# Kernel optimization log

Hardware: AMD Instinct MI355X
Metric: run time of the kernel (lower is better)

## Reference

```python
import jax, jax.numpy as jnp
import numpy as np

B, L, D, K = 16, 512, 512, 8
D2 = 2 * D
KS = 9
PAD = (KS - 1) // 2
EPS = 1e-5


def _conv_block(x, w, b, g, beta):
    # x: [B, L, D]; conv over time dim with 'same' padding, then LayerNorm over D, ReLU
    y = jax.lax.conv_general_dilated(
        x.transpose(0, 2, 1), w, window_strides=(1,), padding=[(PAD, PAD)],
        dimension_numbers=('NCH', 'OIH', 'NCH'))
    y = y.transpose(0, 2, 1) + b  # [B, L, D]
    mean = jnp.mean(y, axis=-1, keepdims=True)
    var = jnp.var(y, axis=-1, keepdims=True)
    y = (y - mean) * jax.lax.rsqrt(var + EPS) * g + beta
    return jax.nn.relu(y)


def _gru_scan(x, w_ih, w_hh, b_ih, b_hh):
    # x: [B, L, D]; torch GRUCell math, input = concat(x_t, h_{t-1}) per module
    def step(h, x_t):
        p = jnp.concatenate([x_t, h], axis=-1)          # [B, D + D2]
        gi = p @ w_ih.T + b_ih                          # [B, 3*D2]
        gh = h @ w_hh.T + b_hh
        ir, iz, inn = jnp.split(gi, 3, axis=-1)
        hr, hz, hn = jnp.split(gh, 3, axis=-1)
        r = jax.nn.sigmoid(ir + hr)
        z = jax.nn.sigmoid(iz + hz)
        n = jnp.tanh(inn + r * hn)
        h_new = (1.0 - z) * n + z * h
        return h_new, h_new

    h0 = jnp.zeros((x.shape[0], w_hh.shape[1]), x.dtype)
    _, hs = jax.lax.scan(step, h0, x.transpose(1, 0, 2))  # [L, B, D2]
    return hs.transpose(1, 0, 2)                           # [B, L, D2]


def setup_inputs() -> dict:
    key = jax.random.key(0)
    ks = jax.random.split(key, 12)
    n = lambda k, sh, s=0.02: jax.random.normal(k, sh, dtype=jnp.float32) * s
    return {
        'h_text': jax.random.normal(ks[0], (B, L, D), dtype=jnp.float32),
        'conv1_w': n(ks[1], (D, D, KS)), 'conv1_b': jnp.zeros((D,), jnp.float32),
        'ln1_g': jnp.ones((D,), jnp.float32), 'ln1_b': jnp.zeros((D,), jnp.float32),
        'conv2_w': n(ks[2], (D, D, KS)), 'conv2_b': jnp.zeros((D,), jnp.float32),
        'ln2_g': jnp.ones((D,), jnp.float32), 'ln2_b': jnp.zeros((D,), jnp.float32),
        'w_ih': n(ks[3], (3 * D2, D + D2)), 'w_hh': n(ks[4], (3 * D2, D2)),
        'b_ih': jnp.zeros((3 * D2,), jnp.float32), 'b_hh': jnp.zeros((3 * D2,), jnp.float32),
        'mdn_w_w': n(ks[5], (K, D2)), 'mdn_w_b': jnp.zeros((K,), jnp.float32),
        'mdn_sigma_w': n(ks[6], (K * D2, D2)), 'mdn_sigma_b': jnp.zeros((K * D2,), jnp.float32),
        'mdn_mu_w': n(ks[7], (K * D2, D2)), 'mdn_mu_b': jnp.zeros((K * D2,), jnp.float32),
    }


def reference(h_text, conv1_w, conv1_b, ln1_g, ln1_b, conv2_w, conv2_b, ln2_g, ln2_b,
              w_ih, w_hh, b_ih, b_hh, mdn_w_w, mdn_w_b, mdn_sigma_w, mdn_sigma_b,
              mdn_mu_w, mdn_mu_b):
    x = _conv_block(h_text, conv1_w, conv1_b, ln1_g, ln1_b)
    x = _conv_block(x, conv2_w, conv2_b, ln2_g, ln2_b)
    h = _gru_scan(x, w_ih, w_hh, b_ih, b_hh)                 # [B, L, 2D]
    w = jax.nn.softmax(h @ mdn_w_w.T + mdn_w_b, axis=-1)     # [B, L, K]
    sigma = jnp.exp(h @ mdn_sigma_w.T + mdn_sigma_b).reshape(B, L, K, D2)
    mu = (h @ mdn_mu_w.T + mdn_mu_b).reshape(B, L, K, D2)
    return (w, sigma, mu)
```

## Files before the change

kernel.cpp:

```cpp
#include <hip/hip_runtime.h>
#include <hip/hip_bf16.h>
#include <math.h>

#define BB 16
#define LL 512
#define DD 512
#define DD2 1024
#define KMIX 8
#define LPAD 520
#define GRU_KSTEPS 33

typedef __attribute__((ext_vector_type(8))) short short8;
typedef __attribute__((ext_vector_type(4))) float f32x4;
typedef unsigned short ushort;

__device__ __forceinline__ float bf2f(ushort u) {
  union { float f; unsigned i; } v; v.i = ((unsigned)u) << 16; return v.f;
}
__device__ __forceinline__ ushort f2bf(float f) {
  union { float f; unsigned i; } v; v.f = f;
  unsigned i = v.i;
  unsigned r = i + 0x7FFF + ((i >> 16) & 1);
  return (ushort)(r >> 16);
}

__global__ void k_zero_bf16(ushort* p, long n) {
  for (long i = blockIdx.x * 256 + threadIdx.x; i < n; i += (long)gridDim.x * 256) p[i] = 0;
}
__global__ void k_fill_xpad(const float* __restrict__ x, ushort* __restrict__ xp) {
  const long n = (long)BB * LPAD * DD;
  for (long i = blockIdx.x * 256 + threadIdx.x; i < n; i += (long)gridDim.x * 256) {
    int d = (int)(i & 511);
    long rest = i >> 9;
    int p = (int)(rest % LPAD);
    int b = (int)(rest / LPAD);
    float v = 0.f;
    if (p >= 4 && p < 516) v = x[((long)b * LL + (p - 4)) * DD + d];
    xp[i] = f2bf(v);
  }
}
__global__ void k_pack_convw(const float* __restrict__ w, ushort* __restrict__ wp) {
  const long n = (long)DD * DD * 9;
  for (long idx = blockIdx.x * 256 + threadIdx.x; idx < n; idx += (long)gridDim.x * 256) {
    int i = (int)(idx & 511);
    int o = (int)((idx >> 9) & 511);
    int k = (int)(idx >> 18);
    wp[idx] = f2bf(w[((long)o * DD + i) * 9 + k]);
  }
}
__global__ void k_pack_wihx(const float* __restrict__ w_ih, ushort* __restrict__ wp) {
  const long n = (long)3 * DD2 * DD;
  for (long idx = blockIdx.x * 256 + threadIdx.x; idx < n; idx += (long)gridDim.x * 256) {
    int i = (int)(idx & 511);
    int nr = (int)(idx >> 9);
    wp[idx] = f2bf(w_ih[(long)nr * 1536 + i]);
  }
}
__global__ void k_pack_bf16(const float* __restrict__ s, ushort* __restrict__ d, long n) {
  for (long i = blockIdx.x * 256 + threadIdx.x; i < n; i += (long)gridDim.x * 256) d[i] = f2bf(s[i]);
}
__global__ void k_pack_gru(const float* __restrict__ w_ih, const float* __restrict__ w_hh,
                           const float* __restrict__ b_hh, ushort* __restrict__ wp) {
  const long n = (long)64 * 6 * GRU_KSTEPS * 64 * 8;
  for (long idx = blockIdx.x * 256 + threadIdx.x; idx < n; idx += (long)gridDim.x * 256) {
    int j = (int)(idx & 7);
    int lane = (int)((idx >> 3) & 63);
    long r9 = idx >> 9;
    int ks = (int)(r9 % GRU_KSTEPS);
    long tmp = r9 / GRU_KSTEPS;
    int s = (int)(tmp % 6);
    int blk = (int)(tmp / 6);
    int k = ks * 32 + ((lane >> 4) << 3) + j;
    int u = blk * 16 + (lane & 15);
    float v = 0.f;
    if (s < 3) {
      if (k < 1024) v = w_ih[((long)(s * DD2 + u)) * 1536 + 512 + k];
    } else {
      int nr = (s - 3) * DD2 + u;
      if (k < 1024) v = w_hh[(long)nr * DD2 + k];
      else if (k == 1024) v = b_hh[nr];
    }
    wp[idx] = f2bf(v);
  }
}
__global__ void k_init_hbuf(ushort* hb, unsigned* flags) {
  int i = blockIdx.x * 256 + threadIdx.x;
  if (i < 16384) hb[i] = 0;
  if (i < 1024) flags[i] = 0u;
}

template <int MODE, int AMAP>
__global__ __launch_bounds__(256) void gemm128(
    const ushort* __restrict__ A, int lda, long segAoff,
    const ushort* __restrict__ Bt, int ldb, long segBoff,
    int nseg, int kseg, void* __restrict__ Cout, int ldc,
    const float* __restrict__ bias) {
  __shared__ ushort As[128 * 64];
  __shared__ ushort Bs[128 * 64];
  const int tid = threadIdx.x, lane = tid & 63, w = tid >> 6;
  const int wr = w >> 1, wc = w & 1;
  const int m0 = blockIdx.y * 128, n0 = blockIdx.x * 128;

  const ushort* Abase;
  if (AMAP == 1) {
    int b = m0 >> 9, l = m0 & 511;
    Abase = A + ((long)(b * LPAD + l)) * DD;
  } else {
    Abase = A + (long)m0 * lda;
  }
  const ushort* Bbase = Bt + (long)n0 * ldb;

  f32x4 acc[4][4];
#pragma unroll
  for (int i = 0; i < 4; i++)
#pragma unroll
    for (int j = 0; j < 4; j++) acc[i][j] = {0.f, 0.f, 0.f, 0.f};

  for (int seg = 0; seg < nseg; ++seg) {
    const ushort* Aseg = Abase + (long)seg * segAoff;
    const ushort* Bseg = Bbase + (long)seg * segBoff;
    for (int k0 = 0; k0 < kseg; k0 += 64) {
#pragma unroll
      for (int it = 0; it < 4; ++it) {
        int chunk = it * 256 + tid;
        int r = chunk >> 3, cc = chunk & 7;
        int sc = cc ^ (r & 7);
        *(short8*)&As[(size_t)chunk * 8] = *(const short8*)(Aseg + (long)r * lda + k0 + sc * 8);
        *(short8*)&Bs[(size_t)chunk * 8] = *(const short8*)(Bseg + (long)r * ldb + k0 + sc * 8);
      }
      __syncthreads();
#pragma unroll
      for (int kk = 0; kk < 2; ++kk) {
        short8 af[4], bfv[4];
#pragma unroll
        for (int m = 0; m < 4; m++) {
          int row = wr * 64 + m * 16 + (lane & 15);
          int ch = (kk * 4 + (lane >> 4)) ^ (row & 7);
          af[m] = *(const short8*)&As[(size_t)(row * 8 + ch) * 8];
        }
#pragma unroll
        for (int nn = 0; nn < 4; nn++) {
          int row = wc * 64 + nn * 16 + (lane & 15);
          int ch = (kk * 4 + (lane >> 4)) ^ (row & 7);
          bfv[nn] = *(const short8*)&Bs[(size_t)(row * 8 + ch) * 8];
        }
#pragma unroll
        for (int m = 0; m < 4; m++)
#pragma unroll
          for (int nn = 0; nn < 4; nn++)
            acc[m][nn] = __builtin_amdgcn_mfma_f32_16x16x32_bf16(af[m], bfv[nn], acc[m][nn], 0, 0, 0);
      }
      __syncthreads();
    }
  }
  float bvals[4];
#pragma unroll
  for (int nn = 0; nn < 4; nn++) {
    int c = n0 + wc * 64 + nn * 16 + (lane & 15);
    bvals[nn] = bias[c];
  }
#pragma unroll
  for (int m = 0; m < 4; m++) {
    int rbase = m0 + wr * 64 + m * 16 + ((lane >> 4) << 2);
#pragma unroll
    for (int nn = 0; nn < 4; nn++) {
      int c = n0 + wc * 64 + nn * 16 + (lane & 15);
#pragma unroll
      for (int j = 0; j < 4; j++) {
        float v = acc[m][nn][j] + bvals[nn];
        long off = (long)(rbase + j) * ldc + c;
        if (MODE == 0) ((float*)Cout)[off] = v;
        else if (MODE == 1) ((ushort*)Cout)[off] = f2bf(v);
        else if (MODE == 2) ((float*)Cout)[off] = v;
        else if (MODE == 3) ((float*)Cout)[off] = expf(v);
        else {
          int r = rbase + j;
          int bb = r >> 9, tt = r & 511, ss = c >> 10, uu = c & 1023;
          long o2 = ((((long)(tt * 64 + (uu >> 4))) * 3 + ss) << 8) + (bb << 4) + (uu & 15);
          ((ushort*)Cout)[o2] = f2bf(v);
        }
      }
    }
  }
}

template <int DSTPAD>
__global__ __launch_bounds__(256) void ln_relu(
    const float* __restrict__ y, const float* __restrict__ g,
    const float* __restrict__ be, ushort* __restrict__ dst) {
  const int r = blockIdx.x, tid = threadIdx.x;
  float v0 = y[(long)r * DD + tid];
  float v1 = y[(long)r * DD + 256 + tid];
  float s = v0 + v1, sq = v0 * v0 + v1 * v1;
#pragma unroll
  for (int o = 32; o; o >>= 1) { s += __shfl_down(s, o); sq += __shfl_down(sq, o); }
  __shared__ float red[8];
  int w = tid >> 6, lane = tid & 63;
  if (lane == 0) { red[w] = s; red[4 + w] = sq; }
  __syncthreads();
  if (tid == 0) {
    float ts = 0.f, tq = 0.f;
#pragma unroll
    for (int i = 0; i < 4; i++) { ts += red[i]; tq += red[4 + i]; }
    red[0] = ts; red[1] = tq;
  }
  __syncthreads();
  float mean = red[0] * (1.f / 512.f);
  float var = red[1] * (1.f / 512.f) - mean * mean;
  float rs = rsqrtf(var + 1e-5f);
  long dbase;
  if (DSTPAD) { int b = r >> 9, l = r & 511; dbase = ((long)(b * LPAD + l + 4)) * DD; }
  else dbase = (long)r * DD;
  float o0 = fmaxf(0.f, (v0 - mean) * rs * g[tid] + be[tid]);
  float o1 = fmaxf(0.f, (v1 - mean) * rs * g[tid + 256] + be[tid + 256]);
  dst[dbase + tid] = f2bf(o0);
  dst[dbase + 256 + tid] = f2bf(o1);
}

__global__ __launch_bounds__(512, 1) void gru_scan(
    const ushort* __restrict__ Wp, const ushort* __restrict__ gix2,
    const float* __restrict__ b_hh,
    ushort* __restrict__ hbuf, ushort* __restrict__ h_seq,
    unsigned* __restrict__ flags) {
  __shared__ float red[8 * 6 * 256];
  const int tid = threadIdx.x, lane = tid & 63, w = tid >> 6, blk = blockIdx.x;
  const int j_c = w;
  const int u_local = lane & 15;
  const int b = ((lane >> 4) << 2) + (j_c & 3);
  const int u = (blk << 4) + u_local;
  const int lanep = ((blk & 1) * 2 + (u_local >> 3)) * 16 + b;
  const long hout_off = ((long)(blk >> 1) * 64 + lanep) * 8 + (u_local & 7);
  const ushort* wpw = Wp + (long)blk * 6 * GRU_KSTEPS * 512 + (long)lane * 8;
  const float bhr = b_hh[u], bhz = b_hh[DD2 + u], bhn = b_hh[2 * DD2 + u];
  float hold = 0.f;

  short8 wr0[4], wr1[4], wr2[4], wr3[4], wr4[4], wr5[4];
#pragma unroll
  for (int i = 0; i < 4; ++i) {
    const int ks = i * 8 + w;
    wr0[i] = *(const short8*)(wpw + (long)(0 * GRU_KSTEPS + ks) * 512);
    wr1[i] = *(const short8*)(wpw + (long)(1 * GRU_KSTEPS + ks) * 512);
    wr2[i] = *(const short8*)(wpw + (long)(2 * GRU_KSTEPS + ks) * 512);
    wr3[i] = *(const short8*)(wpw + (long)(3 * GRU_KSTEPS + ks) * 512);
    wr4[i] = *(const short8*)(wpw + (long)(4 * GRU_KSTEPS + ks) * 512);
    wr5[i] = *(const short8*)(wpw + (long)(5 * GRU_KSTEPS + ks) * 512);
  }

  const int gofs = (b << 4) + u_local;
  for (int t = 0; t < LL; ++t) {
    float gx_r = 0.f, gx_z = 0.f, gx_n = 0.f;
    if (w < 4) {
      const long gbase = ((long)(t * 64 + blk) * 3) << 8;
      gx_r = bf2f(__builtin_nontemporal_load(gix2 + gbase + gofs));
      gx_z = bf2f(__builtin_nontemporal_load(gix2 + gbase + 256 + gofs));
      gx_n = bf2f(__builtin_nontemporal_load(gix2 + gbase + 512 + gofs));
    }

    if (t > 0) {
      if (w == 0) {
        const unsigned tgt = (unsigned)t;
        while (1) {
          unsigned f = __hip_atomic_load(&flags[lane << 4], __ATOMIC_RELAXED,
                                         __HIP_MEMORY_SCOPE_AGENT);
          if (__all((int)(f >= tgt))) break;
          __builtin_amdgcn_s_sleep(1);
        }
      }
      __syncthreads();
    }

    const ushort* hb = hbuf + ((long)t << 14);
    f32x4 acc0 = {0.f,0.f,0.f,0.f}, acc1 = acc0, acc2 = acc0,
          acc3 = acc0, acc4 = acc0, acc5 = acc0;
#pragma unroll
    for (int i = 0; i < 4; ++i) {
      const int ks = i * 8 + w;
      unsigned long long* ap = (unsigned long long*)(hb + (((long)ks * 64 + lane) << 3));
      union { unsigned long long q[2]; short8 v; } cv;
      cv.q[0] = __hip_atomic_load(ap,     __ATOMIC_RELAXED, __HIP_MEMORY_SCOPE_AGENT);
      cv.q[1] = __hip_atomic_load(ap + 1, __ATOMIC_RELAXED, __HIP_MEMORY_SCOPE_AGENT);
      acc0 = __builtin_amdgcn_mfma_f32_16x16x32_bf16(cv.v, wr0[i], acc0, 0, 0, 0);
      acc1 = __builtin_amdgcn_mfma_f32_16x16x32_bf16(cv.v, wr1[i], acc1, 0, 0, 0);
      acc2 = __builtin_amdgcn_mfma_f32_16x16x32_bf16(cv.v, wr2[i], acc2, 0, 0, 0);
      acc3 = __builtin_amdgcn_mfma_f32_16x16x32_bf16(cv.v, wr3[i], acc3, 0, 0, 0);
      acc4 = __builtin_amdgcn_mfma_f32_16x16x32_bf16(cv.v, wr4[i], acc4, 0, 0, 0);
      acc5 = __builtin_amdgcn_mfma_f32_16x16x32_bf16(cv.v, wr5[i], acc5, 0, 0, 0);
    }
#pragma unroll
    for (int j = 0; j < 4; ++j) {
      red[((w * 6 + 0) << 8) + (j << 6) + lane] = acc0[j];
      red[((w * 6 + 1) << 8) + (j << 6) + lane] = acc1[j];
      red[((w * 6 + 2) << 8) + (j << 6) + lane] = acc2[j];
      red[((w * 6 + 3) << 8) + (j << 6) + lane] = acc3[j];
      red[((w * 6 + 4) << 8) + (j << 6) + lane] = acc4[j];
      red[((w * 6 + 5) << 8) + (j << 6) + lane] = acc5[j];
    }
    __syncthreads();
    ushort h16 = 0;
    if (w < 4) {
      float v0 = 0.f, v1 = 0.f, v2 = 0.f, v3 = 0.f, v4 = 0.f, v5 = 0.f;
#pragma unroll
      for (int wv = 0; wv < 8; ++wv) {
        const int base = ((wv * 6) << 8) + (j_c << 6) + lane;
        v0 += red[base];
        v1 += red[base + 256];
        v2 += red[base + 512];
        v3 += red[base + 768];
        v4 += red[base + 1024];
        v5 += red[base + 1280];
      }
      const float rg = 1.f / (1.f + __expf(-(gx_r + v0 + v3 + bhr)));
      const float zg = 1.f / (1.f + __expf(-(gx_z + v1 + v4 + bhz)));
      const float nx = gx_n + v2 + rg * (v5 + bhn);
      const float ng = 1.f - 2.f / (__expf(2.f * nx) + 1.f);
      const float hn = (1.f - zg) * ng + zg * hold;
      hold = hn;
      h16 = f2bf(hn);
    }
    if (t < LL - 1) {
      if (w < 4)
        __hip_atomic_store(hbuf + (((long)(t + 1)) << 14) + hout_off, h16,
                           __ATOMIC_RELAXED, __HIP_MEMORY_SCOPE_AGENT);
      __syncthreads();
      if (tid == 0)
        __hip_atomic_store(&flags[blk << 4], (unsigned)(t + 1), __ATOMIC_RELAXED,
                           __HIP_MEMORY_SCOPE_AGENT);
    }
    if (w < 4)
      __builtin_nontemporal_store(h16, h_seq + ((long)b * LL + t) * DD2 + u);
  }
}

__global__ __launch_bounds__(256) void w_head(
    const ushort* __restrict__ h_seq, const float* __restrict__ ww,
    const float* __restrict__ wb, float* __restrict__ out) {
  const int tid = threadIdx.x, lane = tid & 63, w = tid >> 6;
  const long r = (long)blockIdx.x * 4 + w;
  float s[KMIX];
#pragma unroll
  for (int k = 0; k < KMIX; k++) s[k] = 0.f;
  for (int u = lane; u < DD2; u += 64) {
    float hv = bf2f(h_seq[r * DD2 + u]);
#pragma unroll
    for (int k = 0; k < KMIX; k++) s[k] += hv * ww[(long)k * DD2 + u];
  }
#pragma unroll
  for (int k = 0; k < KMIX; k++)
#pragma unroll
    for (int o = 32; o; o >>= 1) s[k] += __shfl_xor(s[k], o);
#pragma unroll
  for (int k = 0; k < KMIX; k++) s[k] += wb[k];
  float m = s[0];
#pragma unroll
  for (int k = 1; k < KMIX; k++) m = fmaxf(m, s[k]);
  float esum = 0.f;
#pragma unroll
  for (int k = 0; k < KMIX; k++) { s[k] = expf(s[k] - m); esum += s[k]; }
  float mine = 0.f;
#pragma unroll
  for (int k = 0; k < KMIX; k++) if (lane == k) mine = s[k];
  if (lane < KMIX) out[r * KMIX + lane] = mine / esum;
}

extern "C" void kernel_launch(void* const* d_in, const int* in_sizes, int n_in,
                              void* d_out, int out_size, void* d_ws, size_t ws_size,
                              hipStream_t stream) {
  const float* h_text     = (const float*)d_in[0];
  const float* conv1_w    = (const float*)d_in[1];
  const float* conv1_b    = (const float*)d_in[2];
  const float* ln1_g      = (const float*)d_in[3];
  const float* ln1_b      = (const float*)d_in[4];
  const float* conv2_w    = (const float*)d_in[5];
  const float* conv2_b    = (const float*)d_in[6];
  const float* ln2_g      = (const float*)d_in[7];
  const float* ln2_b      = (const float*)d_in[8];
  const float* w_ih       = (const float*)d_in[9];
  const float* w_hh       = (const float*)d_in[10];
  const float* b_ih       = (const float*)d_in[11];
  const float* b_hh       = (const float*)d_in[12];
  const float* mdn_w_w    = (const float*)d_in[13];
  const float* mdn_w_b    = (const float*)d_in[14];
  const float* mdn_sig_w  = (const float*)d_in[15];
  const float* mdn_sig_b  = (const float*)d_in[16];
  const float* mdn_mu_w   = (const float*)d_in[17];
  const float* mdn_mu_b   = (const float*)d_in[18];
  float* out = (float*)d_out;

  char* ws = (char*)d_ws;
  size_t off = 0;
  auto take = [&](size_t bytes) {
    void* p = ws + off;
    off += (bytes + 255) & ~(size_t)255;
    return p;
  };
  ushort* xpad1  = (ushort*)take((size_t)BB * LPAD * DD * 2);
  ushort* xpad2  = (ushort*)take((size_t)BB * LPAD * DD * 2);
  ushort* wpack1 = (ushort*)take((size_t)DD * DD * 9 * 2);
  ushort* wpack2 = (ushort*)take((size_t)DD * DD * 9 * 2);
  float*  ybuf   = (float*) take((size_t)BB * LL * DD * 4);
  ushort* x2     = (ushort*)take((size_t)BB * LL * DD * 2);
  ushort* wihx   = (ushort*)take((size_t)3 * DD2 * DD * 2);
  ushort* gix    = (ushort*)take((size_t)BB * LL * 3 * DD2 * 2);
  ushort* Wp     = (ushort*)take((size_t)64 * 6 * GRU_KSTEPS * 64 * 8 * 2);
  ushort* hseq   = (ushort*)take((size_t)BB * LL * DD2 * 2);
  ushort* mdnmu  = (ushort*)take((size_t)KMIX * DD2 * DD2 * 2);
  ushort* mdnsg  = (ushort*)take((size_t)KMIX * DD2 * DD2 * 2);
  ushort* hbuf   = (ushort*)take((size_t)512 * 16384 * 2);
  unsigned* flags = (unsigned*)take(64 * 16 * 4);

  const long sigma_off = (long)BB * LL * KMIX;
  const long mu_off    = sigma_off + (long)BB * LL * KMIX * DD2;

  k_fill_xpad<<<2048, 256, 0, stream>>>(h_text, xpad1);
  k_zero_bf16<<<2048, 256, 0, stream>>>(xpad2, (long)BB * LPAD * DD);
  k_pack_convw<<<2048, 256, 0, stream>>>(conv1_w, wpack1);
  k_pack_convw<<<2048, 256, 0, stream>>>(conv2_w, wpack2);
  k_pack_wihx<<<2048, 256, 0, stream>>>(w_ih, wihx);
  k_pack_gru<<<2048, 256, 0, stream>>>(w_ih, w_hh, b_hh, Wp);
  k_pack_bf16<<<2048, 256, 0, stream>>>(mdn_mu_w, mdnmu, (long)KMIX * DD2 * DD2);
  k_pack_bf16<<<2048, 256, 0, stream>>>(mdn_sig_w, mdnsg, (long)KMIX * DD2 * DD2);
  k_init_hbuf<<<64, 256, 0, stream>>>(hbuf, flags);

  gemm128<0, 1><<<dim3(4, 64), 256, 0, stream>>>(xpad1, DD, DD, wpack1, DD, (long)DD * DD, 9, DD,
                                                 ybuf, DD, conv1_b);
  ln_relu<1><<<BB * LL, 256, 0, stream>>>(ybuf, ln1_g, ln1_b, xpad2);

  gemm128<0, 1><<<dim3(4, 64), 256, 0, stream>>>(xpad2, DD, DD, wpack2, DD, (long)DD * DD, 9, DD,
                                                 ybuf, DD, conv2_b);
  ln_relu<0><<<BB * LL, 256, 0, stream>>>(ybuf, ln2_g, ln2_b, x2);

  gemm128<4, 0><<<dim3(24, 64), 256, 0, stream>>>(x2, DD, 0, wihx, DD, 0, 1, DD,
                                                  gix, 3 * DD2, b_ih);

  gru_scan<<<64, 512, 0, stream>>>(Wp, gix, b_hh, hbuf, hseq, flags);

  gemm128<3, 0><<<dim3(64, 64), 256, 0, stream>>>(hseq, DD2, 0, mdnsg, DD2, 0, 1, DD2,
                                                  out + sigma_off, KMIX * DD2, mdn_sig_b);
  gemm128<2, 0><<<dim3(64, 64), 256, 0, stream>>>(hseq, DD2, 0, mdnmu, DD2, 0, 1, DD2,
                                                  out + mu_off, KMIX * DD2, mdn_mu_b);
  w_head<<<BB * LL / 4, 256, 0, stream>>>(hseq, mdn_w_w, mdn_w_b, out);
}
```

Before: 1.932 ms.

## Overlap MDN sigma/mu GEMMs with GRU scan in a persistent fused kernel

Merges the GRU recurrence and the MDN sigma/mu projections into one 256-block kernel. 64 blocks run the scan while the other blocks wait on per-timestep flags and compute 128-row chunks of both projections as soon as those hidden states exist. Each chunk loads the shared A tile once for both weight matrices. This hides most of the projection GEMM time behind the latency-bound scan. The cost is contention for CUs and memory bandwidth with the scan blocks, plus reliance on all 256 blocks being co-resident so the spin waits cannot deadlock.

```diff
diff --git a/kernel.cpp b/kernel.cpp
--- a/kernel.cpp
+++ b/kernel.cpp
@@ -170,9 +170,6 @@
         float v = acc[m][nn][j] + bvals[nn];
         long off = (long)(rbase + j) * ldc + c;
         if (MODE == 0) ((float*)Cout)[off] = v;
-        else if (MODE == 1) ((ushort*)Cout)[off] = f2bf(v);
-        else if (MODE == 2) ((float*)Cout)[off] = v;
-        else if (MODE == 3) ((float*)Cout)[off] = expf(v);
         else {
           int r = rbase + j;
           int bb = r >> 9, tt = r & 511, ss = c >> 10, uu = c & 1023;
@@ -217,117 +214,234 @@
   dst[dbase + 256 + tid] = f2bf(o1);
 }
 
-__global__ __launch_bounds__(512, 1) void gru_scan(
+__device__ __forceinline__ void wait_flags(unsigned need, int tid,
+                                           const unsigned* __restrict__ flags) {
+  if ((tid >> 6) == 0) {
+    while (1) {
+      unsigned f = __hip_atomic_load(&flags[(tid & 63) << 4], __ATOMIC_RELAXED,
+                                     __HIP_MEMORY_SCOPE_AGENT);
+      if (__all((int)(f >= need))) break;
+      __builtin_amdgcn_s_sleep(32);
+    }
+  }
+  __syncthreads();
+}
+
+__device__ void do_pair(int m0, int n0,
+                        const ushort* __restrict__ A,
+                        const ushort* __restrict__ Bsg, const ushort* __restrict__ Bmu,
+                        const float* __restrict__ sg_b, const float* __restrict__ mu_b,
+                        float* __restrict__ Cs, float* __restrict__ Cm,
+                        char* smem, int tid) {
+  ushort* As = (ushort*)smem;
+  ushort* B1 = As + 128 * 64;
+  ushort* B2 = B1 + 128 * 64;
+  const int lane = tid & 63, w = tid >> 6;
+  const int wr = w >> 2, wc = w & 3;
+  const ushort* Abase = A + (long)m0 * DD2;
+  const ushort* Bsb = Bsg + (long)n0 * DD2;
+  const ushort* Bmb = Bmu + (long)n0 * DD2;
+  f32x4 accS[4][2], accM[4][2];
+#pragma unroll
+  for (int m = 0; m < 4; m++)
+#pragma unroll
+    for (int n = 0; n < 2; n++) { accS[m][n] = {0.f,0.f,0.f,0.f}; accM[m][n] = {0.f,0.f,0.f,0.f}; }
+
+  for (int k0 = 0; k0 < DD2; k0 += 64) {
+#pragma unroll
+    for (int it = 0; it < 2; ++it) {
+      int chunk = it * 512 + tid;
+      int r = chunk >> 3, cc = chunk & 7, sc = cc ^ (r & 7);
+      *(short8*)&As[(size_t)chunk * 8] = *(const short8*)(Abase + (long)r * DD2 + k0 + sc * 8);
+      *(short8*)&B1[(size_t)chunk * 8] = *(const short8*)(Bsb + (long)r * DD2 + k0 + sc * 8);
+      *(short8*)&B2[(size_t)chunk * 8] = *(const short8*)(Bmb + (long)r * DD2 + k0 + sc * 8);
+    }
+    __syncthreads();
+#pragma unroll
+    for (int kk = 0; kk < 2; ++kk) {
+      short8 af[4], b1[2], b2[2];
+#pragma unroll
+      for (int m = 0; m < 4; m++) {
+        int row = wr * 64 + m * 16 + (lane & 15);
+        int ch = (kk * 4 + (lane >> 4)) ^ (row & 7);
+        af[m] = *(const short8*)&As[(size_t)(row * 8 + ch) * 8];
+      }
+#pragma unroll
+      for (int n = 0; n < 2; n++) {
+        int row = wc * 32 + n * 16 + (lane & 15);
+        int ch = (kk * 4 + (lane >> 4)) ^ (row & 7);
+        b1[n] = *(const short8*)&B1[(size_t)(row * 8 + ch) * 8];
+        b2[n] = *(const short8*)&B2[(size_t)(row * 8 + ch) * 8];
+      }
+#pragma unroll
+      for (int m = 0; m < 4; m++)
+#pragma unroll
+        for (int n = 0; n < 2; n++) {
+          accS[m][n] = __builtin_amdgcn_mfma_f32_16x16x32_bf16(af[m], b1[n], accS[m][n], 0, 0, 0);
+          accM[m][n] = __builtin_amdgcn_mfma_f32_16x16x32_bf16(af[m], b2[n], accM[m][n], 0, 0, 0);
+        }
+    }
+    __syncthreads();
+  }
+  const int ldc = KMIX * DD2;
+#pragma unroll
+  for (int n = 0; n < 2; n++) {
+    const int c = n0 + wc * 32 + n * 16 + (lane & 15);
+    const float bs = sg_b[c], bm = mu_b[c];
+#pragma unroll
+    for (int m = 0; m < 4; m++) {
+      const int rbase = m0 + wr * 64 + m * 16 + ((lane >> 4) << 2);
+#pragma unroll
+      for (int j = 0; j < 4; j++) {
+        const long off = (long)(rbase + j) * ldc + c;
+        Cs[off] = expf(accS[m][n][j] + bs);
+        Cm[off] = accM[m][n][j] + bm;
+      }
+    }
+  }
+}
+
+__global__ __launch_bounds__(512, 4) void fused_scan_mdn(
     const ushort* __restrict__ Wp, const ushort* __restrict__ gix2,
     const float* __restrict__ b_hh,
     ushort* __restrict__ hbuf, ushort* __restrict__ h_seq,
-    unsigned* __restrict__ flags) {
-  __shared__ float red[8 * 6 * 256];
-  const int tid = threadIdx.x, lane = tid & 63, w = tid >> 6, blk = blockIdx.x;
-  const int j_c = w;
-  const int u_local = lane & 15;
-  const int b = ((lane >> 4) << 2) + (j_c & 3);
-  const int u = (blk << 4) + u_local;
-  const int lanep = ((blk & 1) * 2 + (u_local >> 3)) * 16 + b;
-  const long hout_off = ((long)(blk >> 1) * 64 + lanep) * 8 + (u_local & 7);
-  const ushort* wpw = Wp + (long)blk * 6 * GRU_KSTEPS * 512 + (long)lane * 8;
-  const float bhr = b_hh[u], bhz = b_hh[DD2 + u], bhn = b_hh[2 * DD2 + u];
-  float hold = 0.f;
-
-  short8 wr0[4], wr1[4], wr2[4], wr3[4], wr4[4], wr5[4];
-#pragma unroll
-  for (int i = 0; i < 4; ++i) {
-    const int ks = i * 8 + w;
-    wr0[i] = *(const short8*)(wpw + (long)(0 * GRU_KSTEPS + ks) * 512);
-    wr1[i] = *(const short8*)(wpw + (long)(1 * GRU_KSTEPS + ks) * 512);
-    wr2[i] = *(const short8*)(wpw + (long)(2 * GRU_KSTEPS + ks) * 512);
-    wr3[i] = *(const short8*)(wpw + (long)(3 * GRU_KSTEPS + ks) * 512);
-    wr4[i] = *(const short8*)(wpw + (long)(4 * GRU_KSTEPS + ks) * 512);
-    wr5[i] = *(const short8*)(wpw + (long)(5 * GRU_KSTEPS + ks) * 512);
-  }
-
-  const int gofs = (b << 4) + u_local;
-  for (int t = 0; t < LL; ++t) {
-    float gx_r = 0.f, gx_z = 0.f, gx_n = 0.f;
-    if (w < 4) {
-      const long gbase = ((long)(t * 64 + blk) * 3) << 8;
-      gx_r = bf2f(__builtin_nontemporal_load(gix2 + gbase + gofs));
-      gx_z = bf2f(__builtin_nontemporal_load(gix2 + gbase + 256 + gofs));
-      gx_n = bf2f(__builtin_nontemporal_load(gix2 + gbase + 512 + gofs));
-    }
-
-    if (t > 0) {
-      if (w == 0) {
-        const unsigned tgt = (unsigned)t;
-        while (1) {
-          unsigned f = __hip_atomic_load(&flags[lane << 4], __ATOMIC_RELAXED,
-                                         __HIP_MEMORY_SCOPE_AGENT);
-          if (__all((int)(f >= tgt))) break;
-          __builtin_amdgcn_s_sleep(1);
-        }
-      }
-      __syncthreads();
-    }
-
-    const ushort* hb = hbuf + ((long)t << 14);
-    f32x4 acc0 = {0.f,0.f,0.f,0.f}, acc1 = acc0, acc2 = acc0,
-          acc3 = acc0, acc4 = acc0, acc5 = acc0;
+    unsigned* __restrict__ flags,
+    const ushort* __restrict__ mdnsg, const ushort* __restrict__ mdnmu,
+    const float* __restrict__ sg_b, const float* __restrict__ mu_b,
+    float* __restrict__ outS, float* __restrict__ outM) {
+  __shared__ char smem[49152];
+  const int tid = threadIdx.x;
+
+  if (blockIdx.x < 64) {
+    float* red = (float*)smem;
+    const int lane = tid & 63, w = tid >> 6, blk = blockIdx.x;
+    const int j_c = w;
+    const int u_local = lane & 15;
+    const int b = ((lane >> 4) << 2) + (j_c & 3);
+    const int u = (blk << 4) + u_local;
+    const int lanep = ((blk & 1) * 2 + (u_local >> 3)) * 16 + b;
+    const long hout_off = ((long)(blk >> 1) * 64 + lanep) * 8 + (u_local & 7);
+    const ushort* wpw = Wp + (long)blk * 6 * GRU_KSTEPS * 512 + (long)lane * 8;
+    const float bhr = b_hh[u], bhz = b_hh[DD2 + u], bhn = b_hh[2 * DD2 + u];
+    float hold = 0.f;
+
+    short8 wr0[4], wr1[4], wr2[4], wr3[4], wr4[4], wr5[4];
 #pragma unroll
     for (int i = 0; i < 4; ++i) {
       const int ks = i * 8 + w;
-      unsigned long long* ap = (unsigned long long*)(hb + (((long)ks * 64 + lane) << 3));
-      union { unsigned long long q[2]; short8 v; } cv;
-      cv.q[0] = __hip_atomic_load(ap,     __ATOMIC_RELAXED, __HIP_MEMORY_SCOPE_AGENT);
-      cv.q[1] = __hip_atomic_load(ap + 1, __ATOMIC_RELAXED, __HIP_MEMORY_SCOPE_AGENT);
-      acc0 = __builtin_amdgcn_mfma_f32_16x16x32_bf16(cv.v, wr0[i], acc0, 0, 0, 0);
-      acc1 = __builtin_amdgcn_mfma_f32_16x16x32_bf16(cv.v, wr1[i], acc1, 0, 0, 0);
-      acc2 = __builtin_amdgcn_mfma_f32_16x16x32_bf16(cv.v, wr2[i], acc2, 0, 0, 0);
-      acc3 = __builtin_amdgcn_mfma_f32_16x16x32_bf16(cv.v, wr3[i], acc3, 0, 0, 0);
-      acc4 = __builtin_amdgcn_mfma_f32_16x16x32_bf16(cv.v, wr4[i], acc4, 0, 0, 0);
-      acc5 = __builtin_amdgcn_mfma_f32_16x16x32_bf16(cv.v, wr5[i], acc5, 0, 0, 0);
-    }
-#pragma unroll
-    for (int j = 0; j < 4; ++j) {
-      red[((w * 6 + 0) << 8) + (j << 6) + lane] = acc0[j];
-      red[((w * 6 + 1) << 8) + (j << 6) + lane] = acc1[j];
-      red[((w * 6 + 2) << 8) + (j << 6) + lane] = acc2[j];
-      red[((w * 6 + 3) << 8) + (j << 6) + lane] = acc3[j];
-      red[((w * 6 + 4) << 8) + (j << 6) + lane] = acc4[j];
-      red[((w * 6 + 5) << 8) + (j << 6) + lane] = acc5[j];
+      wr0[i] = *(const short8*)(wpw + (long)(0 * GRU_KSTEPS + ks) * 512);
+      wr1[i] = *(const short8*)(wpw + (long)(1 * GRU_KSTEPS + ks) * 512);
+      wr2[i] = *(const short8*)(wpw + (long)(2 * GRU_KSTEPS + ks) * 512);
+      wr3[i] = *(const short8*)(wpw + (long)(3 * GRU_KSTEPS + ks) * 512);
+      wr4[i] = *(const short8*)(wpw + (long)(4 * GRU_KSTEPS + ks) * 512);
+      wr5[i] = *(const short8*)(wpw + (long)(5 * GRU_KSTEPS + ks) * 512);
+    }
+
+    const int gofs = (b << 4) + u_local;
+    for (int t = 0; t < LL; ++t) {
+      float gx_r = 0.f, gx_z = 0.f, gx_n = 0.f;
+      if (w < 4) {
+        const long gbase = ((long)(t * 64 + blk) * 3) << 8;
+        gx_r = bf2f(__builtin_nontemporal_load(gix2 + gbase + gofs));
+        gx_z = bf2f(__builtin_nontemporal_load(gix2 + gbase + 256 + gofs));
+        gx_n = bf2f(__builtin_nontemporal_load(gix2 + gbase + 512 + gofs));
+      }
+      if (t > 0) {
+        if (w == 0) {
+          const unsigned tgt = (unsigned)t;
+          while (1) {
+            unsigned f = __hip_atomic_load(&flags[lane << 4], __ATOMIC_RELAXED,
+                                           __HIP_MEMORY_SCOPE_AGENT);
+            if (__all((int)(f >= tgt))) break;
+            __builtin_amdgcn_s_sleep(1);
+          }
+        }
+        __syncthreads();
+      }
+
+      const ushort* hb = hbuf + ((long)t << 14);
+      f32x4 acc0 = {0.f,0.f,0.f,0.f}, acc1 = acc0, acc2 = acc0,
+            acc3 = acc0, acc4 = acc0, acc5 = acc0;
+#pragma unroll
+      for (int i = 0; i < 4; ++i) {
+        const int ks = i * 8 + w;
+        unsigned long long* ap = (unsigned long long*)(hb + (((long)ks * 64 + lane) << 3));
+        union { unsigned long long q[2]; short8 v; } cv;
+        cv.q[0] = __hip_atomic_load(ap,     __ATOMIC_RELAXED, __HIP_MEMORY_SCOPE_AGENT);
+        cv.q[1] = __hip_atomic_load(ap + 1, __ATOMIC_RELAXED, __HIP_MEMORY_SCOPE_AGENT);
+        acc0 = __builtin_amdgcn_mfma_f32_16x16x32_bf16(cv.v, wr0[i], acc0, 0, 0, 0);
+        acc1 = __builtin_amdgcn_mfma_f32_16x16x32_bf16(cv.v, wr1[i], acc1, 0, 0, 0);
+        acc2 = __builtin_amdgcn_mfma_f32_16x16x32_bf16(cv.v, wr2[i], acc2, 0, 0, 0);
+        acc3 = __builtin_amdgcn_mfma_f32_16x16x32_bf16(cv.v, wr3[i], acc3, 0, 0, 0);
+        acc4 = __builtin_amdgcn_mfma_f32_16x16x32_bf16(cv.v, wr4[i], acc4, 0, 0, 0);
+        acc5 = __builtin_amdgcn_mfma_f32_16x16x32_bf16(cv.v, wr5[i], acc5, 0, 0, 0);
+      }
+#pragma unroll
+      for (int j = 0; j < 4; ++j) {
+        red[((w * 6 + 0) << 8) + (j << 6) + lane] = acc0[j];
+        red[((w * 6 + 1) << 8) + (j << 6) + lane] = acc1[j];
+        red[((w * 6 + 2) << 8) + (j << 6) + lane] = acc2[j];
+        red[((w * 6 + 3) << 8) + (j << 6) + lane] = acc3[j];
+        red[((w * 6 + 4) << 8) + (j << 6) + lane] = acc4[j];
+        red[((w * 6 + 5) << 8) + (j << 6) + lane] = acc5[j];
+      }
+      __syncthreads();
+      ushort h16 = 0;
+      if (w < 4) {
+        float v0 = 0.f, v1 = 0.f, v2 = 0.f, v3 = 0.f, v4 = 0.f, v5 = 0.f;
+#pragma unroll
+        for (int wv = 0; wv < 8; ++wv) {
+          const int base = ((wv * 6) << 8) + (j_c << 6) + lane;
+          v0 += red[base];
+          v1 += red[base + 256];
+          v2 += red[base + 512];
+          v3 += red[base + 768];
+          v4 += red[base + 1024];
+          v5 += red[base + 1280];
+        }
+        const float rg = 1.f / (1.f + __expf(-(gx_r + v0 + v3 + bhr)));
+        const float zg = 1.f / (1.f + __expf(-(gx_z + v1 + v4 + bhz)));
+        const float nx = gx_n + v2 + rg * (v5 + bhn);
+        const float ng = 1.f - 2.f / (__expf(2.f * nx) + 1.f);
+        const float hn = (1.f - zg) * ng + zg * hold;
+        hold = hn;
+        h16 = f2bf(hn);
+      }
+      if (t < LL - 1) {
+        if (w < 4)
+          __hip_atomic_store(hbuf + (((long)(t + 1)) << 14) + hout_off, h16,
+                             __ATOMIC_RELAXED, __HIP_MEMORY_SCOPE_AGENT);
+        __syncthreads();
+        if (tid == 0)
+          __hip_atomic_store(&flags[blk << 4], (unsigned)(t + 1), __ATOMIC_RELAXED,
+                             __HIP_MEMORY_SCOPE_AGENT);
+      }
+      if (w < 4)
+        __hip_atomic_store(h_seq + ((long)b * LL + t) * DD2 + u, h16,
+                           __ATOMIC_RELAXED, __HIP_MEMORY_SCOPE_AGENT);
     }
     __syncthreads();
-    ushort h16 = 0;
-    if (w < 4) {
-      float v0 = 0.f, v1 = 0.f, v2 = 0.f, v3 = 0.f, v4 = 0.f, v5 = 0.f;
-#pragma unroll
-      for (int wv = 0; wv < 8; ++wv) {
-        const int base = ((wv * 6) << 8) + (j_c << 6) + lane;
-        v0 += red[base];
-        v1 += red[base + 256];
-        v2 += red[base + 512];
-        v3 += red[base + 768];
-        v4 += red[base + 1024];
-        v5 += red[base + 1280];
-      }
-      const float rg = 1.f / (1.f + __expf(-(gx_r + v0 + v3 + bhr)));
-      const float zg = 1.f / (1.f + __expf(-(gx_z + v1 + v4 + bhz)));
-      const float nx = gx_n + v2 + rg * (v5 + bhn);
-      const float ng = 1.f - 2.f / (__expf(2.f * nx) + 1.f);
-      const float hn = (1.f - zg) * ng + zg * hold;
-      hold = hn;
-      h16 = f2bf(hn);
-    }
-    if (t < LL - 1) {
-      if (w < 4)
-        __hip_atomic_store(hbuf + (((long)(t + 1)) << 14) + hout_off, h16,
-                           __ATOMIC_RELAXED, __HIP_MEMORY_SCOPE_AGENT);
-      __syncthreads();
-      if (tid == 0)
-        __hip_atomic_store(&flags[blk << 4], (unsigned)(t + 1), __ATOMIC_RELAXED,
-                           __HIP_MEMORY_SCOPE_AGENT);
-    }
-    if (w < 4)
-      __builtin_nontemporal_store(h16, h_seq + ((long)b * LL + t) * DD2 + u);
+    if (tid == 0)
+      __hip_atomic_store(&flags[blk << 4], 600u, __ATOMIC_RELAXED,
+                         __HIP_MEMORY_SCOPE_AGENT);
+  } else {
+    const int wid = blockIdx.x - 64;
+    for (int i = wid; i < 3072; i += 192) {
+      const int nb = i & 63;
+      const int rest = i >> 6;
+      const int b = rest & 15;
+      const int t0 = (rest >> 4) * 128;
+      wait_flags((unsigned)(t0 + 129), tid, flags);
+      do_pair(b * 512 + t0, nb * 128, h_seq, mdnsg, mdnmu, sg_b, mu_b,
+              outS, outM, smem, tid);
+    }
+  }
+  for (int i = blockIdx.x; i < 1024; i += 256) {
+    const int nb = i & 63;
+    const int b = (i >> 6) & 15;
+    wait_flags(513u, tid, flags);
+    do_pair(b * 512 + 384, nb * 128, h_seq, mdnsg, mdnmu, sg_b, mu_b,
+            outS, outM, smem, tid);
   }
 }
 
@@ -432,11 +546,9 @@
   gemm128<4, 0><<<dim3(24, 64), 256, 0, stream>>>(x2, DD, 0, wihx, DD, 0, 1, DD,
                                                   gix, 3 * DD2, b_ih);
 
-  gru_scan<<<64, 512, 0, stream>>>(Wp, gix, b_hh, hbuf, hseq, flags);
-
-  gemm128<3, 0><<<dim3(64, 64), 256, 0, stream>>>(hseq, DD2, 0, mdnsg, DD2, 0, 1, DD2,
-                                                  out + sigma_off, KMIX * DD2, mdn_sig_b);
-  gemm128<2, 0><<<dim3(64, 64), 256, 0, stream>>>(hseq, DD2, 0, mdnmu, DD2, 0, 1, DD2,
-                                                  out + mu_off, KMIX * DD2, mdn_mu_b);
+  fused_scan_mdn<<<256, 512, 0, stream>>>(Wp, gix, b_hh, hbuf, hseq, flags,
+                                          mdnsg, mdnmu, mdn_sig_b, mdn_mu_b,
+                                          out + sigma_off, out + mu_off);
+
   w_head<<<BB * LL / 4, 256, 0, stream>>>(hseq, mdn_w_w, mdn_w_b, out);
 }
```

Measured after the change: 3.154 ms. 63.2% more time.
